# Optimization experiments

Measured on AMD Instinct MI355X. Metric: run time of the kernel, lower is better.

## Reference

```python
import jax, jax.numpy as jnp
import numpy as np


def setup_inputs() -> dict:
    key = jax.random.key(0)
    ks = jax.random.split(key, 5)
    B, I, H = 16384, 1024, 1024
    return {
        "input": jax.random.normal(ks[0], (B, I), dtype=jnp.float32),
        "h_prev": jax.random.normal(ks[1], (B, H), dtype=jnp.float32),
        "c_prev": jax.random.normal(ks[2], (B, H), dtype=jnp.float32),
        "W_ih": jax.random.normal(ks[3], (4 * H, I), dtype=jnp.float32),
        "W_hh": jax.random.normal(ks[4], (4 * H, H), dtype=jnp.float32),
        "b_ih": jnp.zeros((4 * H,), dtype=jnp.float32),
        "b_hh": jnp.zeros((4 * H,), dtype=jnp.float32),
    }


def reference(input, h_prev, c_prev, W_ih, W_hh, b_ih, b_hh):
    H = h_prev.shape[1]
    gi = input @ W_ih.T + b_ih          # [B, 4H]
    gh = h_prev @ W_hh.T + b_hh         # [B, 4H]
    g = gi + gh
    # chunk order in source: input_gate, forget_gate, candidate, output_gate
    i_g = jax.nn.sigmoid(g[:, 0 * H:1 * H])
    f_g = jax.nn.sigmoid(g[:, 1 * H:2 * H])
    cand = jnp.tanh(g[:, 2 * H:3 * H])
    o_g = jax.nn.sigmoid(g[:, 3 * H:4 * H])
    c_new = c_prev * f_g + i_g * cand
    h_new = jnp.tanh(c_new) * o_g
    return (h_new, c_new)
```

## Files before the change

kernel.cpp:

```cpp
#include <hip/hip_runtime.h>
#include <cstdint>
#include <cstddef>


typedef _Float16 half8 __attribute__((ext_vector_type(8)));
typedef float f32x4 __attribute__((ext_vector_type(4)));

__device__ __forceinline__ float sigmoidf_(float x) { return 1.0f / (1.0f + __expf(-x)); }
__device__ __forceinline__ float tanh_fast(float x) { return 2.0f / (1.0f + __expf(-2.0f * x)) - 1.0f; }

__device__ __forceinline__ void gld16(const void* g, void* lds) {
    __builtin_amdgcn_global_load_lds((const __attribute__((address_space(1))) uint32_t*)g,
                                     (__attribute__((address_space(3))) uint32_t*)lds, 16, 0, 0);
}

__global__ __launch_bounds__(256)
void convert_to_f16(const float* __restrict__ X, const float* __restrict__ H,
                    const float* __restrict__ Wih, const float* __restrict__ Whh,
                    _Float16* __restrict__ ws, long nX, long nW)
{
    long e = ((long)blockIdx.x * 256 + threadIdx.x) * 8;
    long total = 2 * nX + 2 * nW;
    if (e >= total) return;
    const float* src; long off;
    if (e < nX)              { src = X;   off = e; }
    else if (e < 2 * nX)     { src = H;   off = e - nX; }
    else if (e < 2 * nX + nW){ src = Wih; off = e - 2 * nX; }
    else                     { src = Whh; off = e - 2 * nX - nW; }
    float4 a = *(const float4*)(src + off);
    float4 b = *(const float4*)(src + off + 4);
    half8 h;
    h[0]=(_Float16)a.x; h[1]=(_Float16)a.y; h[2]=(_Float16)a.z; h[3]=(_Float16)a.w;
    h[4]=(_Float16)b.x; h[5]=(_Float16)b.y; h[6]=(_Float16)b.z; h[7]=(_Float16)b.w;
    *(half8*)(ws + e) = h;
}

__global__ __launch_bounds__(512, 2)
void lstm_mfma_v5(const _Float16* __restrict__ ws,
                  const float* __restrict__ Cprev,
                  const float* __restrict__ bih, const float* __restrict__ bhh,
                  float* __restrict__ Out, int Btot, int mblocks)
{
    __shared__ alignas(16) char smem[131072];

    const long nX = (long)Btot * 1024;
    const long nW = 4096L * 1024;
    const _Float16* Xh = ws;
    const _Float16* Hh = ws + nX;
    const _Float16* Wi = ws + 2 * nX;
    const _Float16* Wh = ws + 2 * nX + nW;

    const int tid = threadIdx.x;
    const int w = tid >> 6, l = tid & 63;
    const int lr = l & 15, q = l >> 4;
    const int wm = w >> 2, wn = w & 3;

    const int nwg = gridDim.x;
    int bx = blockIdx.x;
    if ((nwg & 7) == 0) bx = (bx & 7) * (nwg >> 3) + (bx >> 3);
    const int hblk = (bx & 15) * 64;
    const int m0   = (bx >> 4) * 256;

    uint32_t gA[2], gB[2], ub[2];
    #pragma unroll
    for (int j = 0; j < 2; ++j) {
        uint32_t u = (uint32_t)(j * 8192 + w * 1024);
        ub[j] = u;
        uint32_t off = u + (uint32_t)l * 16u;
        uint32_t r  = off >> 6;
        uint32_t c  = ((off >> 4) & 3u) ^ ((r >> 1) & 3u);
        gA[j] = (uint32_t)(m0 + (int)r) * 1024u + c * 8u;
        uint32_t gate = (r >> 4) & 3u;
        uint32_t hsub = (r >> 6) * 16u + (r & 15u);
        gB[j] = (gate * 1024u + (uint32_t)hblk + hsub) * 1024u + c * 8u;
    }

    const int sw = (lr >> 1) & 3;
    const int ck = (q ^ sw) * 16;
    const uint32_t aB0 = (uint32_t)((wm * 128 + lr) * 64 + ck);
    const uint32_t bB0 = (uint32_t)((wn * 64  + lr) * 64 + ck);

    f32x4 acc[8][4];
    #pragma unroll
    for (int i = 0; i < 8; ++i)
        #pragma unroll
        for (int j = 0; j < 4; ++j)
            acc[i][j] = (f32x4){0.f, 0.f, 0.f, 0.f};

    auto stage = [&](int ts, int sb) {
        const _Float16* Ap = (ts < 32) ? Xh : Hh;
        const _Float16* Bp = (ts < 32) ? Wi : Wh;
        const uint32_t k0 = (uint32_t)(ts & 31) * 32u;
        char* bA = smem + sb * 16384;
        char* bB = smem + 65536 + sb * 16384;
        gld16(Ap + gA[0] + k0, bA + ub[0]);
        gld16(Ap + gA[1] + k0, bA + ub[1]);
        gld16(Bp + gB[0] + k0, bB + ub[0]);
        gld16(Bp + gB[1] + k0, bB + ub[1]);
    };

    half8 afA[4], bfA[4], agA[4];
    half8 afB[4], bfB[4], agB[4];

    stage(0, 0); stage(1, 1); stage(2, 2);
    asm volatile("s_waitcnt vmcnt(4)" ::: "memory");
    __builtin_amdgcn_s_barrier();
    #pragma unroll
    for (int i = 0; i < 4; ++i) bfA[i] = *(const half8*)(smem + 65536 + bB0 + i * 1024);
    #pragma unroll
    for (int i = 0; i < 4; ++i) afA[i] = *(const half8*)(smem + aB0 + i * 1024);
    #pragma unroll
    for (int i = 0; i < 4; ++i) agA[i] = *(const half8*)(smem + aB0 + (i + 4) * 1024);

#define TILE_HALF(T, CAF, CBF, CAG, NAF, NBF, NAG)                                   \
    {                                                                                \
        const int t_ = (T);                                                          \
        int ts_ = t_ + 3; if (ts_ > 63) ts_ = 63;                                    \
        stage(ts_, (t_ + 3) & 3);                                                    \
        const char* sAn = smem + ((t_ + 1) & 3) * 16384;                             \
        const char* sBn = smem + 65536 + ((t_ + 1) & 3) * 16384;                     \
        _Pragma("unroll")                                                            \
        for (int i = 0; i < 4; ++i) NBF[i] = *(const half8*)(sBn + bB0 + i * 1024);  \
        __builtin_amdgcn_s_setprio(1);                                               \
        _Pragma("unroll")                                                            \
        for (int mt = 0; mt < 4; ++mt)                                               \
            _Pragma("unroll")                                                        \
            for (int nt = 0; nt < 4; ++nt)                                           \
                acc[mt][nt] = __builtin_amdgcn_mfma_f32_16x16x32_f16(CAF[mt], CBF[nt], acc[mt][nt], 0, 0, 0); \
        __builtin_amdgcn_s_setprio(0);                                               \
        _Pragma("unroll")                                                            \
        for (int i = 0; i < 4; ++i) NAF[i] = *(const half8*)(sAn + aB0 + i * 1024);  \
        __builtin_amdgcn_s_setprio(1);                                               \
        _Pragma("unroll")                                                            \
        for (int mt = 0; mt < 4; ++mt)                                               \
            _Pragma("unroll")                                                        \
            for (int nt = 0; nt < 4; ++nt)                                           \
                acc[mt + 4][nt] = __builtin_amdgcn_mfma_f32_16x16x32_f16(CAG[mt], CBF[nt], acc[mt + 4][nt], 0, 0, 0); \
        __builtin_amdgcn_s_setprio(0);                                               \
        _Pragma("unroll")                                                            \
        for (int i = 0; i < 4; ++i) NAG[i] = *(const half8*)(sAn + aB0 + (i + 4) * 1024); \
        asm volatile("s_waitcnt vmcnt(4)" ::: "memory");                             \
        __builtin_amdgcn_s_barrier();                                                \
    }

    #pragma unroll 1
    for (int p = 0; p < 32; ++p) {
        TILE_HALF(2 * p,     afA, bfA, agA, afB, bfB, agB)
        TILE_HALF(2 * p + 1, afB, bfB, agB, afA, bfA, agA)
    }
#undef TILE_HALF
    asm volatile("s_waitcnt vmcnt(0)" ::: "memory");

    const int h = hblk + wn * 16 + lr;
    float bs[4];
    #pragma unroll
    for (int g = 0; g < 4; ++g) bs[g] = bih[g * 1024 + h] + bhh[g * 1024 + h];
    const long c_off = (long)Btot * 1024;
    const int mbase = m0 + wm * 128 + q * 4;

    #pragma unroll
    for (int mt = 0; mt < 8; ++mt) {
        #pragma unroll
        for (int r = 0; r < 4; ++r) {
            const int m = mbase + mt * 16 + r;
            const long idx = (long)m * 1024 + h;
            float gi = acc[mt][0][r] + bs[0];
            float gf = acc[mt][1][r] + bs[1];
            float gc = acc[mt][2][r] + bs[2];
            float go = acc[mt][3][r] + bs[3];
            float ig = sigmoidf_(gi), fg = sigmoidf_(gf);
            float cd = tanh_fast(gc), og = sigmoidf_(go);
            float c_new = Cprev[idx] * fg + ig * cd;
            Out[idx]         = tanh_fast(c_new) * og;
            Out[c_off + idx] = c_new;
        }
    }
}

__global__ __launch_bounds__(256, 2)
void lstm_mfma_f16_fb(const float* __restrict__ X, const float* __restrict__ Hprev,
                      const float* __restrict__ Cprev,
                      const float* __restrict__ Wih, const float* __restrict__ Whh,
                      const float* __restrict__ bih, const float* __restrict__ bhh,
                      float* __restrict__ Out, int Btot, int mblocks)
{
    __shared__ alignas(16) _Float16 As[128][40];
    __shared__ alignas(16) _Float16 Bs[256][40];
    const int tid = threadIdx.x;
    const int w = tid >> 6, lane = tid & 63, lr = lane & 15, q = lane >> 4;
    const int bx = blockIdx.x, mblk = bx % mblocks, nblk = bx / mblocks;
    const int m0 = mblk * 128, hblk = nblk * 64;
    const int sr = tid >> 1, sc = tid & 1;
    f32x4 acc[8][4];
    #pragma unroll
    for (int mt = 0; mt < 8; ++mt)
        #pragma unroll
        for (int g = 0; g < 4; ++g) acc[mt][g] = (f32x4){0.f,0.f,0.f,0.f};
    float4 pa[4], pb0[4], pb1[4];
    const int rb1 = sr + 128;
    const size_t wrow0 = (size_t)((sr >> 6) * 1024 + hblk + (sr & 63)) * 1024;
    const size_t wrow1 = (size_t)((rb1 >> 6) * 1024 + hblk + (rb1 & 63)) * 1024;
    const size_t arow  = (size_t)(m0 + sr) * 1024;
    auto stage_load = [&](int tile) {
        const int phase = tile >> 5;
        const int k0 = (tile & 31) * 32 + sc * 16;
        const float* Ap = phase ? Hprev : X;
        const float* Wp = phase ? Whh : Wih;
        const float4* ap = (const float4*)(Ap + arow + k0);
        const float4* b0 = (const float4*)(Wp + wrow0 + k0);
        const float4* b1 = (const float4*)(Wp + wrow1 + k0);
        #pragma unroll
        for (int i = 0; i < 4; ++i) { pa[i] = ap[i]; pb0[i] = b0[i]; pb1[i] = b1[i]; }
    };
    auto pack8 = [](float4 a, float4 b) {
        half8 h;
        h[0]=(_Float16)a.x; h[1]=(_Float16)a.y; h[2]=(_Float16)a.z; h[3]=(_Float16)a.w;
        h[4]=(_Float16)b.x; h[5]=(_Float16)b.y; h[6]=(_Float16)b.z; h[7]=(_Float16)b.w;
        return h;
    };
    stage_load(0);
    for (int tile = 0; tile < 64; ++tile) {
        __syncthreads();
        *(half8*)&As[sr][sc*16]        = pack8(pa[0], pa[1]);
        *(half8*)&As[sr][sc*16+8]      = pack8(pa[2], pa[3]);
        *(half8*)&Bs[sr][sc*16]        = pack8(pb0[0], pb0[1]);
        *(half8*)&Bs[sr][sc*16+8]      = pack8(pb0[2], pb0[3]);
        *(half8*)&Bs[sr+128][sc*16]    = pack8(pb1[0], pb1[1]);
        *(half8*)&Bs[sr+128][sc*16+8]  = pack8(pb1[2], pb1[3]);
        __syncthreads();
        if (tile + 1 < 64) stage_load(tile + 1);
        half8 bf[4];
        #pragma unroll
        for (int g = 0; g < 4; ++g) bf[g] = *(const half8*)&Bs[g*64 + w*16 + lr][q*8];
        #pragma unroll
        for (int mt = 0; mt < 8; ++mt) {
            half8 a = *(const half8*)&As[mt*16 + lr][q*8];
            #pragma unroll
            for (int g = 0; g < 4; ++g)
                acc[mt][g] = __builtin_amdgcn_mfma_f32_16x16x32_f16(a, bf[g], acc[mt][g], 0, 0, 0);
        }
    }
    const int h = hblk + w * 16 + lr;
    float bs0 = bih[h] + bhh[h];
    float bs1 = bih[1024+h] + bhh[1024+h];
    float bs2 = bih[2048+h] + bhh[2048+h];
    float bs3 = bih[3072+h] + bhh[3072+h];
    const size_t c_off = (size_t)Btot * 1024;
    #pragma unroll
    for (int mt = 0; mt < 8; ++mt)
        #pragma unroll
        for (int r = 0; r < 4; ++r) {
            const int m = m0 + mt*16 + q*4 + r;
            const size_t idx = (size_t)m * 1024 + h;
            float gi = acc[mt][0][r]+bs0, gf = acc[mt][1][r]+bs1;
            float gc = acc[mt][2][r]+bs2, go = acc[mt][3][r]+bs3;
            float ig = sigmoidf_(gi), fg = sigmoidf_(gf);
            float cd = tanh_fast(gc), og = sigmoidf_(go);
            float c_new = Cprev[idx]*fg + ig*cd;
            Out[idx] = tanh_fast(c_new)*og;
            Out[c_off+idx] = c_new;
        }
}

extern "C" void kernel_launch(void* const* d_in, const int* in_sizes, int n_in,
                              void* d_out, int out_size, void* d_ws, size_t ws_size,
                              hipStream_t stream) {
    const float* X     = (const float*)d_in[0];
    const float* Hprev = (const float*)d_in[1];
    const float* Cprev = (const float*)d_in[2];
    const float* Wih   = (const float*)d_in[3];
    const float* Whh   = (const float*)d_in[4];
    const float* bih   = (const float*)d_in[5];
    const float* bhh   = (const float*)d_in[6];
    float* Out = (float*)d_out;

    const int Btot = in_sizes[0] / 1024;
    const long nX = (long)Btot * 1024, nW = 4096L * 1024;
    const size_t need = (size_t)(2 * nX + 2 * nW) * sizeof(_Float16);

    if (ws_size >= need && (Btot % 256) == 0) {
        _Float16* ws = (_Float16*)d_ws;
        const long total = 2 * nX + 2 * nW;
        const int cblocks = (int)((total / 8 + 255) / 256);
        hipLaunchKernelGGL(convert_to_f16, dim3(cblocks), dim3(256), 0, stream,
                           X, Hprev, Wih, Whh, ws, nX, nW);
        const int mblocks = Btot / 256;
        const int nblocks = 1024 / 64;
        hipLaunchKernelGGL(lstm_mfma_v5, dim3(mblocks * nblocks), dim3(512), 0, stream,
                           ws, Cprev, bih, bhh, Out, Btot, mblocks);
    } else {
        const int mblocks = Btot / 128;
        hipLaunchKernelGGL(lstm_mfma_f16_fb, dim3(mblocks * 16), dim3(256), 0, stream,
                           X, Hprev, Cprev, Wih, Whh, bih, bhh, Out, Btot, mblocks);
    }
}
```

Before: 569.2 us.

## Restructure GEMM main loop: split A/B staging, drop register double-buffering

Replaces the register double-buffered fragment prefetch with per-tile LDS fragment loads into one set of registers. Global-to-LDS staging of A and B is now split and interleaved between the two MFMA halves. Extra barriers and lgkmcnt waits are added around each half, and the loop is unrolled by four with constant LDS slot offsets. The aim is to lower register pressure and address arithmetic and to spread the VMEM issue more evenly. The cost is exposed LDS latency before each MFMA block and four barriers per tile instead of one.

```diff
diff --git a/kernel.cpp b/kernel.cpp
--- a/kernel.cpp
+++ b/kernel.cpp
@@ -36,7 +36,7 @@
 }
 
 __global__ __launch_bounds__(512, 2)
-void lstm_mfma_v5(const _Float16* __restrict__ ws,
+void lstm_mfma_v6(const _Float16* __restrict__ ws,
                   const float* __restrict__ Cprev,
                   const float* __restrict__ bih, const float* __restrict__ bhh,
                   float* __restrict__ Out, int Btot, int mblocks)
@@ -77,8 +77,8 @@
 
     const int sw = (lr >> 1) & 3;
     const int ck = (q ^ sw) * 16;
-    const uint32_t aB0 = (uint32_t)((wm * 128 + lr) * 64 + ck);
-    const uint32_t bB0 = (uint32_t)((wn * 64  + lr) * 64 + ck);
+    const char* adA = smem + (uint32_t)((wm * 128 + lr) * 64 + ck);
+    const char* adB = smem + 65536u + (uint32_t)((wn * 64 + lr) * 64 + ck);
 
     f32x4 acc[8][4];
     #pragma unroll
@@ -87,68 +87,71 @@
         for (int j = 0; j < 4; ++j)
             acc[i][j] = (f32x4){0.f, 0.f, 0.f, 0.f};
 
-    auto stage = [&](int ts, int sb) {
+    auto stageA = [&](int ts, int sb) {
         const _Float16* Ap = (ts < 32) ? Xh : Hh;
+        const uint32_t k0 = (uint32_t)(ts & 31) * 32u;
+        char* bA = smem + sb * 16384;
+        gld16(Ap + gA[0] + k0, bA + ub[0]);
+        gld16(Ap + gA[1] + k0, bA + ub[1]);
+    };
+    auto stageB = [&](int ts, int sb) {
         const _Float16* Bp = (ts < 32) ? Wi : Wh;
         const uint32_t k0 = (uint32_t)(ts & 31) * 32u;
-        char* bA = smem + sb * 16384;
         char* bB = smem + 65536 + sb * 16384;
-        gld16(Ap + gA[0] + k0, bA + ub[0]);
-        gld16(Ap + gA[1] + k0, bA + ub[1]);
         gld16(Bp + gB[0] + k0, bB + ub[0]);
         gld16(Bp + gB[1] + k0, bB + ub[1]);
     };
 
-    half8 afA[4], bfA[4], agA[4];
-    half8 afB[4], bfB[4], agB[4];
-
-    stage(0, 0); stage(1, 1); stage(2, 2);
-    asm volatile("s_waitcnt vmcnt(4)" ::: "memory");
+    stageA(0, 0); stageB(0, 0);
+    stageA(1, 1); stageB(1, 1);
+    stageA(2, 2); stageB(2, 2);
+    asm volatile("s_waitcnt vmcnt(8)" ::: "memory");
     __builtin_amdgcn_s_barrier();
-    #pragma unroll
-    for (int i = 0; i < 4; ++i) bfA[i] = *(const half8*)(smem + 65536 + bB0 + i * 1024);
-    #pragma unroll
-    for (int i = 0; i < 4; ++i) afA[i] = *(const half8*)(smem + aB0 + i * 1024);
-    #pragma unroll
-    for (int i = 0; i < 4; ++i) agA[i] = *(const half8*)(smem + aB0 + (i + 4) * 1024);
-
-#define TILE_HALF(T, CAF, CBF, CAG, NAF, NBF, NAG)                                   \
+
+#define TILE(T, SLOT)                                                                \
     {                                                                                \
-        const int t_ = (T);                                                          \
-        int ts_ = t_ + 3; if (ts_ > 63) ts_ = 63;                                    \
-        stage(ts_, (t_ + 3) & 3);                                                    \
-        const char* sAn = smem + ((t_ + 1) & 3) * 16384;                             \
-        const char* sBn = smem + 65536 + ((t_ + 1) & 3) * 16384;                     \
-        _Pragma("unroll")                                                            \
-        for (int i = 0; i < 4; ++i) NBF[i] = *(const half8*)(sBn + bB0 + i * 1024);  \
+        int ts_ = (T) + 3; if (ts_ > 63) ts_ = 63;                                   \
+        const int sb_ = ((T) + 3) & 3;                                               \
+        half8 af[4], bf[4], ag[4];                                                   \
+        _Pragma("unroll")                                                            \
+        for (int i = 0; i < 4; ++i) bf[i] = *(const half8*)(adB + (SLOT) * 16384 + i * 1024); \
+        _Pragma("unroll")                                                            \
+        for (int i = 0; i < 4; ++i) af[i] = *(const half8*)(adA + (SLOT) * 16384 + i * 1024); \
+        stageA(ts_, sb_);                                                            \
+        __builtin_amdgcn_s_barrier();                                                \
+        asm volatile("s_waitcnt lgkmcnt(0)" ::: "memory");                           \
         __builtin_amdgcn_s_setprio(1);                                               \
         _Pragma("unroll")                                                            \
         for (int mt = 0; mt < 4; ++mt)                                               \
             _Pragma("unroll")                                                        \
             for (int nt = 0; nt < 4; ++nt)                                           \
-                acc[mt][nt] = __builtin_amdgcn_mfma_f32_16x16x32_f16(CAF[mt], CBF[nt], acc[mt][nt], 0, 0, 0); \
+                acc[mt][nt] = __builtin_amdgcn_mfma_f32_16x16x32_f16(af[mt], bf[nt], acc[mt][nt], 0, 0, 0); \
         __builtin_amdgcn_s_setprio(0);                                               \
-        _Pragma("unroll")                                                            \
-        for (int i = 0; i < 4; ++i) NAF[i] = *(const half8*)(sAn + aB0 + i * 1024);  \
+        __builtin_amdgcn_s_barrier();                                                \
+        _Pragma("unroll")                                                            \
+        for (int i = 0; i < 4; ++i) ag[i] = *(const half8*)(adA + (SLOT) * 16384 + (i + 4) * 1024); \
+        stageB(ts_, sb_);                                                            \
+        __builtin_amdgcn_s_barrier();                                                \
+        asm volatile("s_waitcnt lgkmcnt(0)" ::: "memory");                           \
         __builtin_amdgcn_s_setprio(1);                                               \
         _Pragma("unroll")                                                            \
         for (int mt = 0; mt < 4; ++mt)                                               \
             _Pragma("unroll")                                                        \
             for (int nt = 0; nt < 4; ++nt)                                           \
-                acc[mt + 4][nt] = __builtin_amdgcn_mfma_f32_16x16x32_f16(CAG[mt], CBF[nt], acc[mt + 4][nt], 0, 0, 0); \
+                acc[mt + 4][nt] = __builtin_amdgcn_mfma_f32_16x16x32_f16(ag[mt], bf[nt], acc[mt + 4][nt], 0, 0, 0); \
         __builtin_amdgcn_s_setprio(0);                                               \
-        _Pragma("unroll")                                                            \
-        for (int i = 0; i < 4; ++i) NAG[i] = *(const half8*)(sAn + aB0 + (i + 4) * 1024); \
-        asm volatile("s_waitcnt vmcnt(4)" ::: "memory");                             \
+        asm volatile("s_waitcnt vmcnt(8)" ::: "memory");                             \
         __builtin_amdgcn_s_barrier();                                                \
     }
 
     #pragma unroll 1
-    for (int p = 0; p < 32; ++p) {
-        TILE_HALF(2 * p,     afA, bfA, agA, afB, bfB, agB)
-        TILE_HALF(2 * p + 1, afB, bfB, agB, afA, bfA, agA)
-    }
-#undef TILE_HALF
+    for (int p = 0; p < 16; ++p) {
+        TILE(4 * p + 0, 0)
+        TILE(4 * p + 1, 1)
+        TILE(4 * p + 2, 2)
+        TILE(4 * p + 3, 3)
+    }
+#undef TILE
     asm volatile("s_waitcnt vmcnt(0)" ::: "memory");
 
     const int h = hblk + wn * 16 + lr;
@@ -286,7 +289,7 @@
                            X, Hprev, Wih, Whh, ws, nX, nW);
         const int mblocks = Btot / 256;
         const int nblocks = 1024 / 64;
-        hipLaunchKernelGGL(lstm_mfma_v5, dim3(mblocks * nblocks), dim3(512), 0, stream,
+        hipLaunchKernelGGL(lstm_mfma_v6, dim3(mblocks * nblocks), dim3(512), 0, stream,
                            ws, Cprev, bih, bhh, Out, Btot, mblocks);
     } else {
         const int mblocks = Btot / 128;
```

Measured after the change: 553.2 us. 1.03x faster.
